# Kernel tuning notes

Hardware: AMD Instinct MI355X
Metric: run time of the kernel (lower is better)

Reference implementation:

```python
import jax, jax.numpy as jnp
import numpy as np

B, N_IN, N_H, N_OUT = 128, 256, 256, 256


def _bimul(W, X):
    # MatrixBiMul: bilinear map W X W^T, W: [out, in], X: [b, in, in] -> [b, out, out]
    return jnp.einsum('oi,bij,qj->boq', W, X, W)


def setup_inputs() -> dict:
    key = jax.random.key(0)
    ks = jax.random.split(key, 12)
    s_in = 1.0 / np.sqrt(N_IN)
    s_h = 1.0 / np.sqrt(N_H)
    return {
        'input': jax.random.normal(ks[0], (B, N_IN, N_IN), jnp.float32),
        'hidden': jax.random.normal(ks[1], (B, N_H, N_H), jnp.float32),
        'cell': jax.random.normal(ks[2], (B, N_H, N_H), jnp.float32),
        'W_fx': jax.random.normal(ks[3], (N_H, N_IN), jnp.float32) * s_in,
        'W_ix': jax.random.normal(ks[4], (N_H, N_IN), jnp.float32) * s_in,
        'W_ox': jax.random.normal(ks[5], (N_OUT, N_IN), jnp.float32) * s_in,
        'W_gx': jax.random.normal(ks[6], (N_H, N_IN), jnp.float32) * s_in,
        'W_fh': jax.random.normal(ks[7], (N_H, N_H), jnp.float32) * s_h,
        'W_ih': jax.random.normal(ks[8], (N_H, N_H), jnp.float32) * s_h,
        'W_oh': jax.random.normal(ks[9], (N_OUT, N_H), jnp.float32) * s_h,
        'W_gh': jax.random.normal(ks[10], (N_H, N_H), jnp.float32) * s_h,
        'W_oc': jax.random.normal(ks[11], (N_OUT, N_H), jnp.float32) * s_h,
    }


def reference(input, hidden, cell, W_fx, W_ix, W_ox, W_gx, W_fh, W_ih, W_oh, W_gh, W_oc):
    fgate = jax.nn.relu(_bimul(W_fx, input) + _bimul(W_fh, hidden))
    igate = jax.nn.relu(_bimul(W_ix, input) + _bimul(W_ih, hidden))
    ogate = jax.nn.relu(_bimul(W_ox, input) + _bimul(W_oh, hidden))
    ggate = jax.nn.relu(_bimul(W_gx, input) + _bimul(W_gh, hidden))
    c = fgate + cell + igate + ggate  # note: additive, as in source (not fgate*cell)
    h = ogate + jax.nn.relu(_bimul(W_oc, c))
    return (h, c)
```

## Files before the change

### kernel.cpp

```cpp
#include <hip/hip_runtime.h>

typedef __bf16 bf16x8 __attribute__((ext_vector_type(8)));
typedef float f32x4 __attribute__((ext_vector_type(4)));

__device__ __forceinline__ unsigned short f2bf(float f) {
    unsigned int u = __builtin_bit_cast(unsigned int, f);
    u += 0x7fff + ((u >> 16) & 1);
    return (unsigned short)(u >> 16);
}

__device__ __forceinline__ void stage_pair(
    const unsigned short* __restrict__ Ap, int lda,
    const unsigned short* __restrict__ Bp, int ldb,
    unsigned short* lds, int k0, int tid)
{
#pragma unroll
    for (int it = 0; it < 4; ++it) {
        int li = it * 256 + tid;
        int row = li >> 3;
        int sc = ((li & 7) ^ (row & 7)) * 8;
        __builtin_amdgcn_global_load_lds(
            (const __attribute__((address_space(1))) void*)(Ap + (long)row * lda + k0 + sc),
            (__attribute__((address_space(3))) void*)&lds[li * 8], 16, 0, 0);
        __builtin_amdgcn_global_load_lds(
            (const __attribute__((address_space(1))) void*)(Bp + (long)row * ldb + k0 + sc),
            (__attribute__((address_space(3))) void*)&lds[8192 + li * 8], 16, 0, 0);
    }
}

__device__ __forceinline__ void stage_one(
    const unsigned short* __restrict__ Ap, int lda,
    unsigned short* buf, int k0, int tid)
{
#pragma unroll
    for (int it = 0; it < 4; ++it) {
        int li = it * 256 + tid;
        int row = li >> 3;
        int sc = ((li & 7) ^ (row & 7)) * 8;
        __builtin_amdgcn_global_load_lds(
            (const __attribute__((address_space(1))) void*)(Ap + (long)row * lda + k0 + sc),
            (__attribute__((address_space(3))) void*)&buf[li * 8], 16, 0, 0);
    }
}

__device__ __forceinline__ void compute_tile(
    const unsigned short* lds, int lane, int wm, int wn, f32x4 (&acc)[4][4])
{
#pragma unroll
    for (int kk = 0; kk < 2; ++kk) {
        const int cl = kk * 4 + (lane >> 4);
        bf16x8 af[4], bfr[4];
#pragma unroll
        for (int m = 0; m < 4; ++m) {
            int row = wm + m * 16 + (lane & 15);
            af[m] = *(const bf16x8*)&lds[row * 64 + ((cl ^ (row & 7)) * 8)];
        }
#pragma unroll
        for (int n = 0; n < 4; ++n) {
            int row = wn + n * 16 + (lane & 15);
            bfr[n] = *(const bf16x8*)&lds[8192 + row * 64 + ((cl ^ (row & 7)) * 8)];
        }
#pragma unroll
        for (int m = 0; m < 4; ++m)
#pragma unroll
            for (int n = 0; n < 4; ++n)
                acc[m][n] = __builtin_amdgcn_mfma_f32_16x16x32_bf16(af[m], bfr[n], acc[m][n], 0, 0, 0);
    }
}

__device__ __forceinline__ void compute_bsc(
    const unsigned short* bufA, const unsigned short* Sc, int k0,
    int lane, int wm, int wn, f32x4 (&acc)[4][4])
{
#pragma unroll
    for (int kk = 0; kk < 2; ++kk) {
        const int cl = kk * 4 + (lane >> 4);
        bf16x8 af[4], bfr[4];
#pragma unroll
        for (int m = 0; m < 4; ++m) {
            int row = wm + m * 16 + (lane & 15);
            af[m] = *(const bf16x8*)&bufA[row * 64 + ((cl ^ (row & 7)) * 8)];
        }
#pragma unroll
        for (int n = 0; n < 4; ++n) {
            int row = wn + n * 16 + (lane & 15);
            bfr[n] = *(const bf16x8*)&Sc[row * 256 + k0 + ((cl ^ (row & 7)) * 8)];
        }
#pragma unroll
        for (int m = 0; m < 4; ++m)
#pragma unroll
            for (int n = 0; n < 4; ++n)
                acc[m][n] = __builtin_amdgcn_mfma_f32_16x16x32_bf16(af[m], bfr[n], acc[m][n], 0, 0, 0);
    }
}

__device__ __forceinline__ void midbar() {
    __builtin_amdgcn_sched_barrier(0);
    __builtin_amdgcn_s_barrier();
    __builtin_amdgcn_sched_barrier(0);
}
__device__ __forceinline__ void endbar6() {
    asm volatile("s_waitcnt vmcnt(6)" ::: "memory");
    __builtin_amdgcn_sched_barrier(0);
    __builtin_amdgcn_s_barrier();
    __builtin_amdgcn_sched_barrier(0);
}
__device__ __forceinline__ void endbar0() {
    asm volatile("s_waitcnt vmcnt(0)" ::: "memory");
    __builtin_amdgcn_sched_barrier(0);
    __builtin_amdgcn_s_barrier();
    __builtin_amdgcn_sched_barrier(0);
}

__global__ __launch_bounds__(256)
void cvt_all(const float* __restrict__ X, const float* __restrict__ H,
             unsigned short* __restrict__ XHb,
             const float* __restrict__ fx, const float* __restrict__ ix,
             const float* __restrict__ ox, const float* __restrict__ gx,
             const float* __restrict__ fh, const float* __restrict__ ih,
             const float* __restrict__ oh, const float* __restrict__ gh,
             const float* __restrict__ oc,
             unsigned short* __restrict__ Wcat, unsigned short* __restrict__ Wocb)
{
    int bid = blockIdx.x;
    if (bid < 8192) {
        long e = ((long)bid * 256 + threadIdx.x) * 8;
        const float* s = (e < 8388608) ? (X + e) : (H + (e - 8388608));
        float4 a = *(const float4*)s;
        float4 c = *(const float4*)(s + 4);
        uint4 uv;
        uv.x = (unsigned)f2bf(a.x) | ((unsigned)f2bf(a.y) << 16);
        uv.y = (unsigned)f2bf(a.z) | ((unsigned)f2bf(a.w) << 16);
        uv.z = (unsigned)f2bf(c.x) | ((unsigned)f2bf(c.y) << 16);
        uv.w = (unsigned)f2bf(c.z) | ((unsigned)f2bf(c.w) << 16);
        *(uint4*)&XHb[e] = uv;
    } else {
        int idx = (bid - 8192) * 256 + threadIdx.x;
        if (idx < 524288) {
            int g = idx >> 17;
            int rem = idx & 131071;
            int q = rem >> 9;
            int j = rem & 511;
            const float* xs = (g == 0) ? fx : (g == 1) ? ix : (g == 2) ? ox : gx;
            const float* hs = (g == 0) ? fh : (g == 1) ? ih : (g == 2) ? oh : gh;
            float v = (j < 256) ? xs[q * 256 + j] : hs[q * 256 + (j - 256)];
            Wcat[idx] = f2bf(v);
        } else if (idx < 589824) {
            int k = idx - 524288;
            Wocb[k] = f2bf(oc[k]);
        }
    }
}

__global__ __launch_bounds__(256)
void gemm_s1(const unsigned short* __restrict__ Wcat,
             const unsigned short* __restrict__ XHb,
             unsigned short* __restrict__ Tcat)
{
    __shared__ alignas(16) unsigned short lds[16384];

    const int tid = threadIdx.x;
    const int lane = tid & 63;
    const int w = tid >> 6;

    int d = blockIdx.x + 4 * blockIdx.y + 512 * blockIdx.z;
    int swz = (d & 7) * 512 + (d >> 3);
    const int x = swz & 3;
    const int b = (swz >> 2) & 127;
    const int gz = swz >> 9;
    const int g = gz >> 1, hf = gz & 1;
    const int tq = (x >> 1) * 128;
    const int ti = (x & 1) * 128;
    const int wm = (w >> 1) * 64;
    const int wn = (w & 1) * 64;

    const unsigned short* Ap = Wcat + (long)g * 131072 + (long)tq * 512 + hf * 256;
    const unsigned short* Bp = XHb + (long)hf * 8388608 + (long)b * 65536 + (long)ti * 256;

    f32x4 acc[4][4];
#pragma unroll
    for (int m = 0; m < 4; ++m)
#pragma unroll
        for (int n = 0; n < 4; ++n)
            acc[m][n] = (f32x4){0.f, 0.f, 0.f, 0.f};

#pragma unroll
    for (int t = 0; t < 4; ++t) {
        if (t > 0) __syncthreads();
        stage_pair(Ap, 512, Bp, 256, lds, t * 64, tid);
        __syncthreads();
        compute_tile(lds, lane, wm, wn, acc);
    }

    unsigned short* Cb = Tcat + (long)g * 16777216 + (long)b * 131072 + hf * 256;
    const int r0 = (lane >> 4) * 4;
    const int c0 = lane & 15;
#pragma unroll
    for (int m = 0; m < 4; ++m)
#pragma unroll
        for (int n = 0; n < 4; ++n)
#pragma unroll
            for (int r = 0; r < 4; ++r) {
                int row = tq + wm + m * 16 + r0 + r;
                int col = ti + wn + n * 16 + c0;
                Cb[(long)row * 512 + col] = f2bf(acc[m][n][r]);
            }
}

__global__ __launch_bounds__(512)
void gemm_gateB8(const unsigned short* __restrict__ Tcat,
                 const unsigned short* __restrict__ Wcat,
                 const float* __restrict__ cell,
                 float* __restrict__ out_c, float* __restrict__ out_h,
                 unsigned short* __restrict__ cb16)
{
    __shared__ alignas(16) unsigned short lds[73728];

    const int tid = threadIdx.x;
    const int lane = tid & 63;
    const int w = tid >> 6;

    int orig = blockIdx.x + 2 * blockIdx.y;
    int swz = (orig & 7) * 32 + (orig >> 3);
    const int b = swz >> 1;
    const int to = (swz & 1) * 128;
    const int wm = (w >> 2) * 64;
    const int wn = (w & 3) * 64;

    const unsigned short* Ab = Wcat + (long)to * 512;
    const unsigned short* Bb = Tcat + (long)b * 131072;

    f32x4 accc[4][4], acc[4][4];
#pragma unroll
    for (int m = 0; m < 4; ++m)
#pragma unroll
        for (int n = 0; n < 4; ++n) {
            accc[m][n] = (f32x4){0.f, 0.f, 0.f, 0.f};
            acc[m][n] = (f32x4){0.f, 0.f, 0.f, 0.f};
        }

    auto stage = [&](int u, int part) {
        int s = u >> 3;
        int gv = s ^ (s >> 1);
        int k0 = (u & 7) * 64;
        const unsigned short* Ap = Ab + (long)gv * 131072;
        const unsigned short* Bp = Bb + (long)gv * 16777216;
        unsigned short* buf = lds + (u % 3) * 24576;
        if (part == 0) {
#pragma unroll
            for (int it = 0; it < 2; ++it) {
                int li = it * 512 + tid;
                int row = li >> 3;
                int sc = ((li & 7) ^ (row & 7)) * 8;
                __builtin_amdgcn_global_load_lds(
                    (const __attribute__((address_space(1))) void*)(Ap + (long)row * 512 + k0 + sc),
                    (__attribute__((address_space(3))) void*)&buf[li * 8], 16, 0, 0);
            }
            {
                int li = tid;
                int row = li >> 3;
                int sc = ((li & 7) ^ (row & 7)) * 8;
                __builtin_amdgcn_global_load_lds(
                    (const __attribute__((address_space(1))) void*)(Bp + (long)row * 512 + k0 + sc),
                    (__attribute__((address_space(3))) void*)&buf[8192 + li * 8], 16, 0, 0);
            }
        } else {
#pragma unroll
            for (int it = 1; it < 4; ++it) {
                int li = it * 512 + tid;
                int row = li >> 3;
                int sc = ((li & 7) ^ (row & 7)) * 8;
                __builtin_amdgcn_global_load_lds(
                    (const __attribute__((address_space(1))) void*)(Bp + (long)row * 512 + k0 + sc),
                    (__attribute__((address_space(3))) void*)&buf[8192 + li * 8], 16, 0, 0);
            }
        }
    };

    auto chalf = [&](const unsigned short* buf, int kk) {
        const int cl = kk * 4 + (lane >> 4);
        bf16x8 af[4], bfr[4];
#pragma unroll
        for (int m = 0; m < 4; ++m) {
            int row = wm + m * 16 + (lane & 15);
            af[m] = *(const bf16x8*)&buf[row * 64 + ((cl ^ (row & 7)) * 8)];
        }
#pragma unroll
        for (int n = 0; n < 4; ++n) {
            int row = wn + n * 16 + (lane & 15);
            bfr[n] = *(const bf16x8*)&buf[8192 + row * 64 + ((cl ^ (row & 7)) * 8)];
        }
        __builtin_amdgcn_s_setprio(1);
#pragma unroll
        for (int m = 0; m < 4; ++m)
#pragma unroll
            for (int n = 0; n < 4; ++n)
                acc[m][n] = __builtin_amdgcn_mfma_f32_16x16x32_bf16(af[m], bfr[n], acc[m][n], 0, 0, 0);
        __builtin_amdgcn_s_setprio(0);
    };

    stage(0, 0); stage(0, 1);
    stage(1, 0); stage(1, 1);
    endbar6();

    for (int u = 0; u < 32; ++u) {
        const unsigned short* cur = lds + (u % 3) * 24576;
        if (u + 2 < 32) stage(u + 2, 0);
        chalf(cur, 0);
        midbar();
        if (u + 2 < 32) stage(u + 2, 1);
        chalf(cur, 1);
        if ((u & 7) == 7 && u != 31) {
#pragma unroll
            for (int m = 0; m < 4; ++m)
#pragma unroll
                for (int n = 0; n < 4; ++n)
#pragma unroll
                    for (int r = 0; r < 4; ++r) {
                        float v = acc[m][n][r];
                        accc[m][n][r] += (v > 0.f ? v : 0.f);
                        acc[m][n][r] = 0.f;
                    }
        }
        if (u < 30) endbar6(); else endbar0();
    }

    const float* cb = cell + (long)b * 65536;
    float* co = out_c + (long)b * 65536;
    float* ho = out_h + (long)b * 65536;
    unsigned short* cbo = cb16 + (long)b * 65536;
    const int r0 = (lane >> 4) * 4;
    const int c0 = lane & 15;
#pragma unroll
    for (int m = 0; m < 4; ++m)
#pragma unroll
        for (int n = 0; n < 4; ++n)
#pragma unroll
            for (int r = 0; r < 4; ++r) {
                int row = to + wm + m * 16 + r0 + r;
                int col = wn + n * 16 + c0;
                long idx = (long)row * 256 + col;
                float cv = accc[m][n][r] + cb[idx];
                co[idx] = cv;
                cbo[idx] = f2bf(cv);
                float v = acc[m][n][r];
                ho[idx] = (v > 0.f ? v : 0.f);
            }
}

__global__ __launch_bounds__(256)
void gemm_woc(const unsigned short* __restrict__ Wocb,
              const unsigned short* __restrict__ cb16,
              float* __restrict__ out_h)
{
    __shared__ alignas(16) unsigned short stg[32768];
    __shared__ alignas(16) unsigned short Sc[32768];

    const int tid = threadIdx.x;
    const int lane = tid & 63;
    const int w = tid >> 6;

    int orig = blockIdx.x + 2 * blockIdx.y;
    int swz = (orig & 7) * 32 + (orig >> 3);
    const int b = swz >> 1;
    const int tq = (swz & 1) * 128;
    const int wm = (w >> 1) * 64;
    const int wn = (w & 1) * 64;
    const int r0 = (lane >> 4) * 4;
    const int c0 = lane & 15;

#pragma unroll
    for (int t2 = 0; t2 < 2; ++t2) {
        const unsigned short* Ap = Wocb + (long)tq * 256;
        const unsigned short* Bp = cb16 + (long)b * 65536 + (long)(t2 * 128) * 256;

        f32x4 acc[4][4];
#pragma unroll
        for (int m = 0; m < 4; ++m)
#pragma unroll
            for (int n = 0; n < 4; ++n)
                acc[m][n] = (f32x4){0.f, 0.f, 0.f, 0.f};

        stage_pair(Ap, 256, Bp, 256, stg, 0, tid);
#pragma unroll
        for (int t = 0; t < 4; ++t) {
            __syncthreads();
            if (t + 1 < 4)
                stage_pair(Ap, 256, Bp, 256, stg + ((t + 1) & 1) * 16384, (t + 1) * 64, tid);
            compute_tile(stg + (t & 1) * 16384, lane, wm, wn, acc);
        }
#pragma unroll
        for (int m = 0; m < 4; ++m)
#pragma unroll
            for (int n = 0; n < 4; ++n)
#pragma unroll
                for (int r = 0; r < 4; ++r) {
                    int qrow = wm + m * 16 + r0 + r;
                    int icol = t2 * 128 + wn + n * 16 + c0;
                    int addr = qrow * 256 + (icol & ~63)
                             + ((((icol >> 3) & 7) ^ (qrow & 7)) * 8) + (icol & 7);
                    Sc[addr] = f2bf(acc[m][n][r]);
                }
    }

    float* ho = out_h + (long)b * 65536;
#pragma unroll
    for (int ot = 0; ot < 2; ++ot) {
        const unsigned short* Ap = Wocb + (long)(ot * 128) * 256;

        f32x4 acc[4][4];
#pragma unroll
        for (int m = 0; m < 4; ++m)
#pragma unroll
            for (int n = 0; n < 4; ++n)
                acc[m][n] = (f32x4){0.f, 0.f, 0.f, 0.f};

        stage_one(Ap, 256, stg, 0, tid);
#pragma unroll
        for (int t = 0; t < 4; ++t) {
            __syncthreads();
            if (t + 1 < 4)
                stage_one(Ap, 256, stg + ((t + 1) & 1) * 16384, (t + 1) * 64, tid);
            compute_bsc(stg + (t & 1) * 16384, Sc, t * 64, lane, wm, wn, acc);
        }
#pragma unroll
        for (int m = 0; m < 4; ++m)
#pragma unroll
            for (int n = 0; n < 4; ++n)
#pragma unroll
                for (int r = 0; r < 4; ++r) {
                    int orow = ot * 128 + wm + m * 16 + r0 + r;
                    int qcol = tq + wn + n * 16 + c0;
                    long idx = (long)orow * 256 + qcol;
                    float v = acc[m][n][r];
                    ho[idx] += (v > 0.f ? v : 0.f);
                }
    }
}

extern "C" void kernel_launch(void* const* d_in, const int* in_sizes, int n_in,
                              void* d_out, int out_size, void* d_ws, size_t ws_size,
                              hipStream_t stream)
{
    (void)in_sizes; (void)n_in; (void)out_size; (void)ws_size;

    const float* X    = (const float*)d_in[0];
    const float* H    = (const float*)d_in[1];
    const float* cell = (const float*)d_in[2];
    const float* Wxp[4] = {(const float*)d_in[3], (const float*)d_in[4],
                           (const float*)d_in[5], (const float*)d_in[6]};
    const float* Whp[4] = {(const float*)d_in[7], (const float*)d_in[8],
                           (const float*)d_in[9], (const float*)d_in[10]};
    const float* Wocf = (const float*)d_in[11];

    float* out_h = (float*)d_out;
    float* out_c = out_h + 8388608;

    unsigned short* ws   = (unsigned short*)d_ws;
    unsigned short* XHb  = ws;
    unsigned short* Wcat = ws + 16777216;
    unsigned short* Wocb = ws + 17301504;
    unsigned short* Tcat = ws + 17367040;
    unsigned short* cb16 = ws + 84475904;

    cvt_all<<<dim3(10496), 256, 0, stream>>>(X, H, XHb,
                                             Wxp[0], Wxp[1], Wxp[2], Wxp[3],
                                             Whp[0], Whp[1], Whp[2], Whp[3],
                                             Wocf, Wcat, Wocb);
    gemm_s1<<<dim3(4, 128, 8), 256, 0, stream>>>(Wcat, XHb, Tcat);
    gemm_gateB8<<<dim3(2, 128), 512, 0, stream>>>(Tcat, Wcat, cell, out_c, out_h, cb16);
    gemm_woc<<<dim3(2, 128), 256, 0, stream>>>(Wocb, cb16, out_h);
}
```

Baseline: 171.2 us.

## Keep input tile resident in LDS across gates and retile gate GEMM

The first-stage GEMM now uses 512-thread blocks. Each block loads its 128-row slice of the bf16 input/hidden tile into LDS once, then streams the four gates' weight slices through a double buffer, writing each gate's result in turn. This removes the repeated reloading of the same activation tile for every gate and output half. The gate GEMM switches from splitting the output rows to splitting the output columns: each block covers all 256 output rows against half of the columns. Its triple-buffered, half-staged pipeline with explicit vmcnt waits and setprio is replaced by a simpler two-buffer loop with a single __syncthreads per step, which reduces LDS use but may expose more load latency.

```diff
diff --git a/kernel.cpp b/kernel.cpp
--- a/kernel.cpp
+++ b/kernel.cpp
@@ -92,24 +92,6 @@
             for (int n = 0; n < 4; ++n)
                 acc[m][n] = __builtin_amdgcn_mfma_f32_16x16x32_bf16(af[m], bfr[n], acc[m][n], 0, 0, 0);
     }
-}
-
-__device__ __forceinline__ void midbar() {
-    __builtin_amdgcn_sched_barrier(0);
-    __builtin_amdgcn_s_barrier();
-    __builtin_amdgcn_sched_barrier(0);
-}
-__device__ __forceinline__ void endbar6() {
-    asm volatile("s_waitcnt vmcnt(6)" ::: "memory");
-    __builtin_amdgcn_sched_barrier(0);
-    __builtin_amdgcn_s_barrier();
-    __builtin_amdgcn_sched_barrier(0);
-}
-__device__ __forceinline__ void endbar0() {
-    asm volatile("s_waitcnt vmcnt(0)" ::: "memory");
-    __builtin_amdgcn_sched_barrier(0);
-    __builtin_amdgcn_s_barrier();
-    __builtin_amdgcn_sched_barrier(0);
 }
 
 __global__ __launch_bounds__(256)
@@ -152,30 +134,55 @@
     }
 }
 
-__global__ __launch_bounds__(256)
-void gemm_s1(const unsigned short* __restrict__ Wcat,
-             const unsigned short* __restrict__ XHb,
-             unsigned short* __restrict__ Tcat)
-{
-    __shared__ alignas(16) unsigned short lds[16384];
+__global__ __launch_bounds__(512)
+void gemm_s1r(const unsigned short* __restrict__ Wcat,
+              const unsigned short* __restrict__ XHb,
+              unsigned short* __restrict__ Tcat)
+{
+    __shared__ alignas(16) unsigned short lds[65536];
 
     const int tid = threadIdx.x;
     const int lane = tid & 63;
     const int w = tid >> 6;
 
-    int d = blockIdx.x + 4 * blockIdx.y + 512 * blockIdx.z;
-    int swz = (d & 7) * 512 + (d >> 3);
-    const int x = swz & 3;
-    const int b = (swz >> 2) & 127;
-    const int gz = swz >> 9;
-    const int g = gz >> 1, hf = gz & 1;
-    const int tq = (x >> 1) * 128;
-    const int ti = (x & 1) * 128;
+    int d = blockIdx.x + 2 * blockIdx.y + 256 * blockIdx.z;
+    int swz = (d & 7) * 64 + (d >> 3);
+    const int ti = (swz & 1) * 128;
+    const int b = (swz >> 1) & 127;
+    const int hf = swz >> 8;
     const int wm = (w >> 1) * 64;
     const int wn = (w & 1) * 64;
 
-    const unsigned short* Ap = Wcat + (long)g * 131072 + (long)tq * 512 + hf * 256;
-    const unsigned short* Bp = XHb + (long)hf * 8388608 + (long)b * 65536 + (long)ti * 256;
+    const unsigned short* Bsrc = XHb + (long)hf * 8388608 + (long)b * 65536 + (long)ti * 256;
+    unsigned short* Bres = lds;
+    unsigned short* Abuf0 = lds + 32768;
+    unsigned short* Abuf1 = lds + 49152;
+
+#pragma unroll
+    for (int it = 0; it < 8; ++it) {
+        int li = it * 512 + tid;
+        int row = li >> 5;
+        int ck = li & 31;
+        int srccol = (ck & ~7) * 8 + (((ck & 7) ^ (row & 7)) * 8);
+        __builtin_amdgcn_global_load_lds(
+            (const __attribute__((address_space(1))) void*)(Bsrc + (long)row * 256 + srccol),
+            (__attribute__((address_space(3))) void*)&Bres[li * 8], 16, 0, 0);
+    }
+
+    auto stageA = [&](int u, unsigned short* buf) {
+        int gate = u >> 2;
+        int t = u & 3;
+        const unsigned short* Ap = Wcat + (long)gate * 131072 + hf * 256 + t * 64;
+#pragma unroll
+        for (int it = 0; it < 4; ++it) {
+            int li = it * 512 + tid;
+            int row = li >> 3;
+            int sc = ((li & 7) ^ (row & 7)) * 8;
+            __builtin_amdgcn_global_load_lds(
+                (const __attribute__((address_space(1))) void*)(Ap + (long)row * 512 + sc),
+                (__attribute__((address_space(3))) void*)&buf[li * 8], 16, 0, 0);
+        }
+    };
 
     f32x4 acc[4][4];
 #pragma unroll
@@ -184,37 +191,41 @@
         for (int n = 0; n < 4; ++n)
             acc[m][n] = (f32x4){0.f, 0.f, 0.f, 0.f};
 
-#pragma unroll
-    for (int t = 0; t < 4; ++t) {
-        if (t > 0) __syncthreads();
-        stage_pair(Ap, 512, Bp, 256, lds, t * 64, tid);
-        __syncthreads();
-        compute_tile(lds, lane, wm, wn, acc);
-    }
-
-    unsigned short* Cb = Tcat + (long)g * 16777216 + (long)b * 131072 + hf * 256;
     const int r0 = (lane >> 4) * 4;
     const int c0 = lane & 15;
-#pragma unroll
-    for (int m = 0; m < 4; ++m)
-#pragma unroll
-        for (int n = 0; n < 4; ++n)
-#pragma unroll
-            for (int r = 0; r < 4; ++r) {
-                int row = tq + wm + m * 16 + r0 + r;
-                int col = ti + wn + n * 16 + c0;
-                Cb[(long)row * 512 + col] = f2bf(acc[m][n][r]);
-            }
+
+    stageA(0, Abuf0);
+    for (int u = 0; u < 16; ++u) {
+        __syncthreads();
+        if (u + 1 < 16) stageA(u + 1, (u & 1) ? Abuf0 : Abuf1);
+        const unsigned short* bufA = (u & 1) ? Abuf1 : Abuf0;
+        compute_bsc(bufA, Bres, (u & 3) * 64, lane, wm, wn, acc);
+        if ((u & 3) == 3) {
+            int gate = u >> 2;
+            unsigned short* Cb = Tcat + (long)gate * 16777216 + (long)b * 131072;
+#pragma unroll
+            for (int m = 0; m < 4; ++m)
+#pragma unroll
+                for (int n = 0; n < 4; ++n)
+#pragma unroll
+                    for (int r = 0; r < 4; ++r) {
+                        int row = wm + m * 16 + r0 + r;
+                        int col = hf * 256 + ti + wn + n * 16 + c0;
+                        Cb[(long)row * 512 + col] = f2bf(acc[m][n][r]);
+                        acc[m][n][r] = 0.f;
+                    }
+        }
+    }
 }
 
 __global__ __launch_bounds__(512)
-void gemm_gateB8(const unsigned short* __restrict__ Tcat,
+void gemm_gateBq(const unsigned short* __restrict__ Tcat,
                  const unsigned short* __restrict__ Wcat,
                  const float* __restrict__ cell,
                  float* __restrict__ out_c, float* __restrict__ out_h,
                  unsigned short* __restrict__ cb16)
 {
-    __shared__ alignas(16) unsigned short lds[73728];
+    __shared__ alignas(16) unsigned short lds[49152];
 
     const int tid = threadIdx.x;
     const int lane = tid & 63;
@@ -223,12 +234,37 @@
     int orig = blockIdx.x + 2 * blockIdx.y;
     int swz = (orig & 7) * 32 + (orig >> 3);
     const int b = swz >> 1;
-    const int to = (swz & 1) * 128;
-    const int wm = (w >> 2) * 64;
-    const int wn = (w & 3) * 64;
-
-    const unsigned short* Ab = Wcat + (long)to * 512;
-    const unsigned short* Bb = Tcat + (long)b * 131072;
+    const int qh = (swz & 1) * 128;
+    const int wm = (w >> 1) * 64;
+    const int wn = (w & 1) * 64;
+
+    const unsigned short* Bb = Tcat + (long)b * 131072 + (long)qh * 512;
+
+    auto stage = [&](int u, unsigned short* buf) {
+        int s = u >> 3;
+        int gv = s ^ (s >> 1);
+        int k0 = (u & 7) * 64;
+        const unsigned short* Ap = Wcat + (long)gv * 131072 + k0;
+        const unsigned short* Bp = Bb + (long)gv * 16777216 + k0;
+#pragma unroll
+        for (int it = 0; it < 4; ++it) {
+            int li = it * 512 + tid;
+            int row = li >> 3;
+            int sc = ((li & 7) ^ (row & 7)) * 8;
+            __builtin_amdgcn_global_load_lds(
+                (const __attribute__((address_space(1))) void*)(Ap + (long)row * 512 + sc),
+                (__attribute__((address_space(3))) void*)&buf[li * 8], 16, 0, 0);
+        }
+#pragma unroll
+        for (int it = 0; it < 2; ++it) {
+            int li = it * 512 + tid;
+            int row = li >> 3;
+            int sc = ((li & 7) ^ (row & 7)) * 8;
+            __builtin_amdgcn_global_load_lds(
+                (const __attribute__((address_space(1))) void*)(Bp + (long)row * 512 + sc),
+                (__attribute__((address_space(3))) void*)&buf[16384 + li * 8], 16, 0, 0);
+        }
+    };
 
     f32x4 accc[4][4], acc[4][4];
 #pragma unroll
@@ -239,77 +275,31 @@
             acc[m][n] = (f32x4){0.f, 0.f, 0.f, 0.f};
         }
 
-    auto stage = [&](int u, int part) {
-        int s = u >> 3;
-        int gv = s ^ (s >> 1);
-        int k0 = (u & 7) * 64;
-        const unsigned short* Ap = Ab + (long)gv * 131072;
-        const unsigned short* Bp = Bb + (long)gv * 16777216;
-        unsigned short* buf = lds + (u % 3) * 24576;
-        if (part == 0) {
-#pragma unroll
-            for (int it = 0; it < 2; ++it) {
-                int li = it * 512 + tid;
-                int row = li >> 3;
-                int sc = ((li & 7) ^ (row & 7)) * 8;
-                __builtin_amdgcn_global_load_lds(
-                    (const __attribute__((address_space(1))) void*)(Ap + (long)row * 512 + k0 + sc),
-                    (__attribute__((address_space(3))) void*)&buf[li * 8], 16, 0, 0);
+    stage(0, lds);
+    for (int u = 0; u < 32; ++u) {
+        __syncthreads();
+        if (u + 1 < 32) stage(u + 1, lds + ((u + 1) & 1) * 24576);
+        const unsigned short* buf = lds + (u & 1) * 24576;
+#pragma unroll
+        for (int kk = 0; kk < 2; ++kk) {
+            const int cl = kk * 4 + (lane >> 4);
+            bf16x8 af[4], bfr[4];
+#pragma unroll
+            for (int m = 0; m < 4; ++m) {
+                int row = wm + m * 16 + (lane & 15);
+                af[m] = *(const bf16x8*)&buf[row * 64 + ((cl ^ (row & 7)) * 8)];
             }
-            {
-                int li = tid;
-                int row = li >> 3;
-                int sc = ((li & 7) ^ (row & 7)) * 8;
-                __builtin_amdgcn_global_load_lds(
-                    (const __attribute__((address_space(1))) void*)(Bp + (long)row * 512 + k0 + sc),
-                    (__attribute__((address_space(3))) void*)&buf[8192 + li * 8], 16, 0, 0);
+#pragma unroll
+            for (int n = 0; n < 4; ++n) {
+                int row = wn + n * 16 + (lane & 15);
+                bfr[n] = *(const bf16x8*)&buf[16384 + row * 64 + ((cl ^ (row & 7)) * 8)];
             }
-        } else {
-#pragma unroll
-            for (int it = 1; it < 4; ++it) {
-                int li = it * 512 + tid;
-                int row = li >> 3;
-                int sc = ((li & 7) ^ (row & 7)) * 8;
-                __builtin_amdgcn_global_load_lds(
-                    (const __attribute__((address_space(1))) void*)(Bp + (long)row * 512 + k0 + sc),
-                    (__attribute__((address_space(3))) void*)&buf[8192 + li * 8], 16, 0, 0);
-            }
-        }
-    };
-
-    auto chalf = [&](const unsigned short* buf, int kk) {
-        const int cl = kk * 4 + (lane >> 4);
-        bf16x8 af[4], bfr[4];
-#pragma unroll
-        for (int m = 0; m < 4; ++m) {
-            int row = wm + m * 16 + (lane & 15);
-            af[m] = *(const bf16x8*)&buf[row * 64 + ((cl ^ (row & 7)) * 8)];
-        }
-#pragma unroll
-        for (int n = 0; n < 4; ++n) {
-            int row = wn + n * 16 + (lane & 15);
-            bfr[n] = *(const bf16x8*)&buf[8192 + row * 64 + ((cl ^ (row & 7)) * 8)];
-        }
-        __builtin_amdgcn_s_setprio(1);
-#pragma unroll
-        for (int m = 0; m < 4; ++m)
-#pragma unroll
-            for (int n = 0; n < 4; ++n)
-                acc[m][n] = __builtin_amdgcn_mfma_f32_16x16x32_bf16(af[m], bfr[n], acc[m][n], 0, 0, 0);
-        __builtin_amdgcn_s_setprio(0);
-    };
-
-    stage(0, 0); stage(0, 1);
-    stage(1, 0); stage(1, 1);
-    endbar6();
-
-    for (int u = 0; u < 32; ++u) {
-        const unsigned short* cur = lds + (u % 3) * 24576;
-        if (u + 2 < 32) stage(u + 2, 0);
-        chalf(cur, 0);
-        midbar();
-        if (u + 2 < 32) stage(u + 2, 1);
-        chalf(cur, 1);
+#pragma unroll
+            for (int m = 0; m < 4; ++m)
+#pragma unroll
+                for (int n = 0; n < 4; ++n)
+                    acc[m][n] = __builtin_amdgcn_mfma_f32_16x16x32_bf16(af[m], bfr[n], acc[m][n], 0, 0, 0);
+        }
         if ((u & 7) == 7 && u != 31) {
 #pragma unroll
             for (int m = 0; m < 4; ++m)
@@ -322,7 +312,6 @@
                         acc[m][n][r] = 0.f;
                     }
         }
-        if (u < 30) endbar6(); else endbar0();
     }
 
     const float* cb = cell + (long)b * 65536;
@@ -337,8 +326,8 @@
         for (int n = 0; n < 4; ++n)
 #pragma unroll
             for (int r = 0; r < 4; ++r) {
-                int row = to + wm + m * 16 + r0 + r;
-                int col = wn + n * 16 + c0;
+                int row = wm + m * 16 + r0 + r;
+                int col = qh + wn + n * 16 + c0;
                 long idx = (long)row * 256 + col;
                 float cv = accc[m][n][r] + cb[idx];
                 co[idx] = cv;
@@ -467,7 +456,7 @@
                                              Wxp[0], Wxp[1], Wxp[2], Wxp[3],
                                              Whp[0], Whp[1], Whp[2], Whp[3],
                                              Wocf, Wcat, Wocb);
-    gemm_s1<<<dim3(4, 128, 8), 256, 0, stream>>>(Wcat, XHb, Tcat);
-    gemm_gateB8<<<dim3(2, 128), 512, 0, stream>>>(Tcat, Wcat, cell, out_c, out_h, cb16);
+    gemm_s1r<<<dim3(2, 128, 2), 512, 0, stream>>>(Wcat, XHb, Tcat);
+    gemm_gateBq<<<dim3(2, 128), 512, 0, stream>>>(Tcat, Wcat, cell, out_c, out_h, cb16);
     gemm_woc<<<dim3(2, 128), 256, 0, stream>>>(Wocb, cb16, out_h);
 }
```

New measurement: 173.8 us. Within noise of the previous version (+1.5%).
